# Kernel optimization log

Measured on AMD Instinct MI355X. Metric: run time of the kernel, lower is better.

## Reference

```python
import jax, jax.numpy as jnp
import numpy as np

N_NODES = 100000
N_EDGES = 1600000
IN_DIM = 128
HID = 128
N_CLS = 10
N_GRAPHS = 128


def setup_inputs() -> dict:
    key = jax.random.key(0)
    ks = jax.random.split(key, 8)
    x = jax.random.normal(ks[0], (N_NODES, IN_DIM), dtype=jnp.float32)
    edge_index = jax.random.randint(ks[1], (2, N_EDGES), 0, N_NODES, dtype=jnp.int64)
    batch = jnp.sort(jax.random.randint(ks[2], (N_NODES,), 0, N_GRAPHS, dtype=jnp.int64))
    # GCNConv weights (PyG uses glorot; scale approximated) and biases
    W1 = jax.random.normal(ks[3], (IN_DIM, HID), dtype=jnp.float32) * (1.0 / np.sqrt(IN_DIM))
    b1 = jnp.zeros((HID,), dtype=jnp.float32)
    W2 = jax.random.normal(ks[4], (HID, HID), dtype=jnp.float32) * (1.0 / np.sqrt(HID))
    b2 = jnp.zeros((HID,), dtype=jnp.float32)
    Wlin = jax.random.normal(ks[5], (HID, N_CLS), dtype=jnp.float32) * (1.0 / np.sqrt(HID))
    blin = jnp.zeros((N_CLS,), dtype=jnp.float32)
    return {"x": x, "edge_index": edge_index, "batch": batch,
            "W1": W1, "b1": b1, "W2": W2, "b2": b2, "Wlin": Wlin, "blin": blin}


def _gcn_norm(edge_index, n_nodes):
    # PyG GCNConv default: add self-loops, symmetric D^-1/2 A D^-1/2 normalization
    loop = jnp.arange(n_nodes, dtype=edge_index.dtype)
    row = jnp.concatenate([edge_index[0], loop])  # source nodes
    col = jnp.concatenate([edge_index[1], loop])  # destination nodes
    ones = jnp.ones(col.shape[0], dtype=jnp.float32)
    deg = jax.ops.segment_sum(ones, col, num_segments=n_nodes)
    dinv = jnp.where(deg > 0, jax.lax.rsqrt(deg), 0.0)
    norm = dinv[row] * dinv[col]  # per-edge normalization coefficient
    return row, col, norm


def _gcn_conv(x, W, b, row, col, norm, n_nodes):
    h = x @ W                                   # [N, hid] dense transform first (small hid)
    msg = h[row] * norm[:, None]                # gather + scale over edges
    out = jax.ops.segment_sum(msg, col, num_segments=n_nodes)  # scatter-add aggregation
    return out + b


def reference(x, edge_index, batch, W1, b1, W2, b2, Wlin, blin):
    n = x.shape[0]
    row, col, norm = _gcn_norm(edge_index, n)
    h = jax.nn.relu(_gcn_conv(x, W1, b1, row, col, norm, n))
    h = jax.nn.relu(_gcn_conv(h, W2, b2, row, col, norm, n))
    # global_mean_pool over batch ids
    sums = jax.ops.segment_sum(h, batch, num_segments=N_GRAPHS)
    cnts = jax.ops.segment_sum(jnp.ones((n,), dtype=h.dtype), batch, num_segments=N_GRAPHS)
    pooled = sums / jnp.maximum(cnts, 1.0)[:, None]
    return pooled @ Wlin + blin  # [N_GRAPHS, n_cls]
```

## Files before the change

kernel.cpp:

```cpp
#include <hip/hip_runtime.h>

#define NN 100000
#define NE 1600000
#define DD 128
#define NG 128
#define NC 10
#define AGG_WAVES 8192

#define B1SH 8
#define NB1 ((NN + 255) / 256)
#define EPB 8192
#define NWG1 ((NE + EPB - 1) / EPB)
#define GEMM_BLOCKS ((NN + 63) / 64)

typedef __attribute__((ext_vector_type(8))) short short8v;
typedef __attribute__((ext_vector_type(4))) float f32x4;

__device__ __forceinline__ unsigned short f2bf(float f) {
    unsigned int u = __float_as_uint(f);
    u = (u + 0x7fffu + ((u >> 16) & 1u)) >> 16;
    return (unsigned short)u;
}
__device__ __forceinline__ float bflo(unsigned int p) { return __uint_as_float(p << 16); }
__device__ __forceinline__ float bfhi(unsigned int p) { return __uint_as_float(p & 0xffff0000u); }

template <int IN_BF16>
__device__ __forceinline__ void gemm_body(const void* __restrict__ Xv,
                                          const unsigned short* __restrict__ Wpk,
                                          const float* __restrict__ dinv,
                                          unsigned short* __restrict__ outb, int blk,
                                          unsigned short* wlds) {
    int tid = threadIdx.x;
    const uint4* wg = (const uint4*)Wpk;
    uint4* wl = (uint4*)wlds;
#pragma unroll
    for (int i = 0; i < 8; ++i) wl[tid + i * 256] = wg[tid + i * 256];
    __syncthreads();

    int w = tid >> 6, lane = tid & 63;
    int kg = lane >> 4;
    int rowbase = blk * 64 + w * 16;
    int rl = min(rowbase + (lane & 15), NN - 1);

    short8v a[4];
    if (IN_BF16) {
        const unsigned short* xb = (const unsigned short*)Xv;
#pragma unroll
        for (int kk = 0; kk < 4; ++kk)
            a[kk] = *(const short8v*)(xb + (long)rl * DD + kk * 32 + kg * 8);
    } else {
        const float* xf = (const float*)Xv;
#pragma unroll
        for (int kk = 0; kk < 4; ++kk) {
            float4 f0 = *(const float4*)(xf + (long)rl * DD + kk * 32 + kg * 8);
            float4 f1 = *(const float4*)(xf + (long)rl * DD + kk * 32 + kg * 8 + 4);
            short8v t;
            t[0] = (short)f2bf(f0.x); t[1] = (short)f2bf(f0.y);
            t[2] = (short)f2bf(f0.z); t[3] = (short)f2bf(f0.w);
            t[4] = (short)f2bf(f1.x); t[5] = (short)f2bf(f1.y);
            t[6] = (short)f2bf(f1.z); t[7] = (short)f2bf(f1.w);
            a[kk] = t;
        }
    }

    f32x4 acc[8];
#pragma unroll
    for (int n = 0; n < 8; ++n) acc[n] = (f32x4){0.f, 0.f, 0.f, 0.f};
#pragma unroll
    for (int n = 0; n < 8; ++n) {
#pragma unroll
        for (int kk = 0; kk < 4; ++kk) {
            short8v b = *(const short8v*)(wlds + ((n * 4 + kk) * 64 + lane) * 8);
            acc[n] = __builtin_amdgcn_mfma_f32_16x16x32_bf16(a[kk], b, acc[n], 0, 0, 0);
        }
    }

    int c0 = lane & 15;
#pragma unroll
    for (int reg = 0; reg < 4; ++reg) {
        int row = rowbase + kg * 4 + reg;
        if (row < NN) {
            float dv = dinv[row];
            unsigned short* op = outb + (long)row * DD + c0;
#pragma unroll
            for (int n = 0; n < 8; ++n) op[n * 16] = f2bf(dv * acc[n][reg]);
        }
    }
}

__global__ __launch_bounds__(256) void k1_fused(const int* __restrict__ col, int* __restrict__ hist,
                                                const float* __restrict__ x,
                                                const unsigned short* __restrict__ Wpk1,
                                                unsigned short* __restrict__ hbuf) {
    __shared__ unsigned short wlds[16384];
    int bid = blockIdx.x, t = threadIdx.x;
    if (bid < NWG1) {
        int* lh = (int*)wlds;
        for (int i = t; i < NB1; i += 256) lh[i] = 0;
        __syncthreads();
        int base = bid * EPB;
        int lim = min(base + EPB, NE);
#pragma unroll 4
        for (int e = base + t; e < lim; e += 256) atomicAdd(&lh[col[e] >> B1SH], 1);
        __syncthreads();
        for (int i = t; i < NB1; i += 256) hist[i * NWG1 + bid] = lh[i];
    } else {
        int tid = threadIdx.x;
        const uint4* wg = (const uint4*)Wpk1;
        uint4* wl = (uint4*)wlds;
#pragma unroll
        for (int i = 0; i < 8; ++i) wl[tid + i * 256] = wg[tid + i * 256];
        __syncthreads();
        int w = tid >> 6, lane = tid & 63;
        int kg = lane >> 4;
        int blk = bid - NWG1;
        int rowbase = blk * 64 + w * 16;
        int rl = min(rowbase + (lane & 15), NN - 1);
        short8v a[4];
        const float* xf = x;
#pragma unroll
        for (int kk = 0; kk < 4; ++kk) {
            float4 f0 = *(const float4*)(xf + (long)rl * DD + kk * 32 + kg * 8);
            float4 f1 = *(const float4*)(xf + (long)rl * DD + kk * 32 + kg * 8 + 4);
            short8v tv;
            tv[0] = (short)f2bf(f0.x); tv[1] = (short)f2bf(f0.y);
            tv[2] = (short)f2bf(f0.z); tv[3] = (short)f2bf(f0.w);
            tv[4] = (short)f2bf(f1.x); tv[5] = (short)f2bf(f1.y);
            tv[6] = (short)f2bf(f1.z); tv[7] = (short)f2bf(f1.w);
            a[kk] = tv;
        }
        f32x4 acc[8];
#pragma unroll
        for (int n = 0; n < 8; ++n) acc[n] = (f32x4){0.f, 0.f, 0.f, 0.f};
#pragma unroll
        for (int n = 0; n < 8; ++n) {
#pragma unroll
            for (int kk = 0; kk < 4; ++kk) {
                short8v b = *(const short8v*)(wlds + ((n * 4 + kk) * 64 + lane) * 8);
                acc[n] = __builtin_amdgcn_mfma_f32_16x16x32_bf16(a[kk], b, acc[n], 0, 0, 0);
            }
        }
        int c0 = lane & 15;
#pragma unroll
        for (int reg = 0; reg < 4; ++reg) {
            int row = rowbase + kg * 4 + reg;
            if (row < NN) {
                unsigned short* op = hbuf + (long)row * DD + c0;
#pragma unroll
                for (int n = 0; n < 8; ++n) op[n * 16] = f2bf(acc[n][reg]);
            }
        }
    }
}

__global__ __launch_bounds__(512) void btot_k(const int* __restrict__ hist, int* __restrict__ bbase) {
    __shared__ int tmp[512];
    int t = threadIdx.x;
    int s = 0;
    if (t < NB1) {
        const int* hp = hist + t * NWG1;
        for (int w = 0; w < NWG1; ++w) s += hp[w];
    }
    tmp[t] = s;
    __syncthreads();
    for (int o = 1; o < 512; o <<= 1) {
        int v = (t >= o) ? tmp[t - o] : 0;
        __syncthreads();
        tmp[t] += v;
        __syncthreads();
    }
    if (t < NB1) bbase[t] = tmp[t] - s;
    if (t == 511) bbase[NB1] = tmp[511];
}

__global__ __launch_bounds__(256) void histscan_k(const int* __restrict__ bbase, int* __restrict__ hist) {
    __shared__ int tmp[256];
    int b = blockIdx.x, t = threadIdx.x;
    int v = (t < NWG1) ? hist[b * NWG1 + t] : 0;
    tmp[t] = v;
    __syncthreads();
    for (int o = 1; o < 256; o <<= 1) {
        int u = (t >= o) ? tmp[t - o] : 0;
        __syncthreads();
        tmp[t] += u;
        __syncthreads();
    }
    int excl = tmp[t] - v;
    if (t < NWG1) hist[b * NWG1 + t] = bbase[b] + excl;
}

__global__ __launch_bounds__(256) void part1_k(const int* __restrict__ row, const int* __restrict__ col,
                                               const int* __restrict__ hist, int* __restrict__ tmpe) {
    __shared__ int lcur[NB1];
    int t = threadIdx.x, w = blockIdx.x;
    for (int i = t; i < NB1; i += 256) lcur[i] = hist[i * NWG1 + w];
    __syncthreads();
    int base = w * EPB;
    int lim = min(base + EPB, NE);
#pragma unroll 4
    for (int e = base + t; e < lim; e += 256) {
        int c = col[e];
        int pos = atomicAdd(&lcur[c >> B1SH], 1);
        tmpe[pos] = (row[e] << B1SH) | (c & 255);
    }
}

__global__ __launch_bounds__(512) void part2b_k(const int* __restrict__ bbase, const int* __restrict__ tmpe,
                                                unsigned int* __restrict__ csr_src, int* __restrict__ offs,
                                                float* __restrict__ dinv, unsigned int* __restrict__ hpb) {
    __shared__ int lcnt[256];
    __shared__ int lsc[256];
    int b = blockIdx.x, t = threadIdx.x;
    if (t < 256) lcnt[t] = 0;
    __syncthreads();
    int ebeg = bbase[b], eend = bbase[b + 1];
    for (int e = ebeg + t; e < eend; e += 512) atomicAdd(&lcnt[tmpe[e] & 255], 1);
    __syncthreads();
    if (t < 256) lsc[t] = lcnt[t];
    __syncthreads();
    for (int o = 1; o < 256; o <<= 1) {
        int v = (t < 256 && t >= o) ? lsc[t - o] : 0;
        __syncthreads();
        if (t < 256) lsc[t] += v;
        __syncthreads();
    }
    int n0 = b << B1SH;
    if (t < 256) {
        int c = lcnt[t];
        int excl = lsc[t] - c;
        int node = n0 + t;
        float dvf = rsqrtf((float)c + 1.0f);
        if (node < NN) {
            offs[node] = ebeg + excl;
            dinv[node] = dvf;
        }
        lsc[t] = ebeg + excl;
        ((float*)lcnt)[t] = dvf;
    }
    if (b == NB1 - 1 && t == 0) offs[NN] = NE;
    __syncthreads();
    for (int e = ebeg + t; e < eend; e += 512) {
        int p = tmpe[e];
        int pos = atomicAdd(&lsc[p & 255], 1);
        csr_src[pos] = (unsigned int)(p >> B1SH) << 6;
    }
    int nend = min(n0 + 256, NN);
    unsigned int lane = t & 63;
    for (int r = n0 + (t >> 6); r < nend; r += 8) {
        float dv = ((const float*)lcnt)[r - n0];
        unsigned int p = hpb[(unsigned int)r * 64u + lane];
        hpb[(unsigned int)r * 64u + lane] =
            ((unsigned int)f2bf(dv * bflo(p))) | ((unsigned int)f2bf(dv * bfhi(p)) << 16);
    }
}

__global__ __launch_bounds__(256) void pack_w2_k(const float* __restrict__ W1, const float* __restrict__ W2,
                                                 unsigned short* __restrict__ Wpk1,
                                                 unsigned short* __restrict__ Wpk2,
                                                 float* __restrict__ gsum) {
    int t = threadIdx.x;
    if (blockIdx.x == 2) {
        float4* g4 = (float4*)gsum;
        for (int i = t; i < NG * DD / 4; i += 256) g4[i] = make_float4(0, 0, 0, 0);
        return;
    }
    const float* W = blockIdx.x ? W2 : W1;
    unsigned short* Wpk = blockIdx.x ? Wpk2 : Wpk1;
    for (int f = t * 64; f < t * 64 + 64; ++f) {
        int j = f & 7, lane = (f >> 3) & 63, kk = (f >> 9) & 3, n = f >> 11;
        int k = kk * 32 + ((lane >> 4) << 3) + j;
        int c = n * 16 + (lane & 15);
        Wpk[f] = f2bf(W[k * DD + c]);
    }
}

__global__ __launch_bounds__(256) void gemm2_k(const unsigned short* __restrict__ xb,
                                               const unsigned short* __restrict__ Wpk,
                                               const float* __restrict__ dinv,
                                               unsigned short* __restrict__ outb) {
    __shared__ unsigned short wlds[16384];
    gemm_body<1>(xb, Wpk, dinv, outb, blockIdx.x, wlds);
}

__device__ __forceinline__ void agg_node(const unsigned int* __restrict__ hpb,
                                         const unsigned int* __restrict__ csr,
                                         int s, int e_end, unsigned int lane,
                                         float& accx, float& accy) {
    int e = s;
    for (; e + 16 <= e_end; e += 16) {
        unsigned int p0 = hpb[csr[e] + lane];
        unsigned int p1 = hpb[csr[e + 1] + lane];
        unsigned int p2 = hpb[csr[e + 2] + lane];
        unsigned int p3 = hpb[csr[e + 3] + lane];
        unsigned int p4 = hpb[csr[e + 4] + lane];
        unsigned int p5 = hpb[csr[e + 5] + lane];
        unsigned int p6 = hpb[csr[e + 6] + lane];
        unsigned int p7 = hpb[csr[e + 7] + lane];
        unsigned int q0 = hpb[csr[e + 8] + lane];
        unsigned int q1 = hpb[csr[e + 9] + lane];
        unsigned int q2 = hpb[csr[e + 10] + lane];
        unsigned int q3 = hpb[csr[e + 11] + lane];
        unsigned int q4 = hpb[csr[e + 12] + lane];
        unsigned int q5 = hpb[csr[e + 13] + lane];
        unsigned int q6 = hpb[csr[e + 14] + lane];
        unsigned int q7 = hpb[csr[e + 15] + lane];
        accx += ((bflo(p0) + bflo(p1)) + (bflo(p2) + bflo(p3))) +
                ((bflo(p4) + bflo(p5)) + (bflo(p6) + bflo(p7))) +
                ((bflo(q0) + bflo(q1)) + (bflo(q2) + bflo(q3))) +
                ((bflo(q4) + bflo(q5)) + (bflo(q6) + bflo(q7)));
        accy += ((bfhi(p0) + bfhi(p1)) + (bfhi(p2) + bfhi(p3))) +
                ((bfhi(p4) + bfhi(p5)) + (bfhi(p6) + bfhi(p7))) +
                ((bfhi(q0) + bfhi(q1)) + (bfhi(q2) + bfhi(q3))) +
                ((bfhi(q4) + bfhi(q5)) + (bfhi(q6) + bfhi(q7)));
    }
    if (e + 8 <= e_end) {
        unsigned int p0 = hpb[csr[e] + lane];
        unsigned int p1 = hpb[csr[e + 1] + lane];
        unsigned int p2 = hpb[csr[e + 2] + lane];
        unsigned int p3 = hpb[csr[e + 3] + lane];
        unsigned int p4 = hpb[csr[e + 4] + lane];
        unsigned int p5 = hpb[csr[e + 5] + lane];
        unsigned int p6 = hpb[csr[e + 6] + lane];
        unsigned int p7 = hpb[csr[e + 7] + lane];
        accx += (bflo(p0) + bflo(p1)) + (bflo(p2) + bflo(p3)) +
                (bflo(p4) + bflo(p5)) + (bflo(p6) + bflo(p7));
        accy += (bfhi(p0) + bfhi(p1)) + (bfhi(p2) + bfhi(p3)) +
                (bfhi(p4) + bfhi(p5)) + (bfhi(p6) + bfhi(p7));
        e += 8;
    }
    if (e + 4 <= e_end) {
        unsigned int p0 = hpb[csr[e] + lane];
        unsigned int p1 = hpb[csr[e + 1] + lane];
        unsigned int p2 = hpb[csr[e + 2] + lane];
        unsigned int p3 = hpb[csr[e + 3] + lane];
        accx += (bflo(p0) + bflo(p1)) + (bflo(p2) + bflo(p3));
        accy += (bfhi(p0) + bfhi(p1)) + (bfhi(p2) + bfhi(p3));
        e += 4;
    }
    for (; e < e_end; ++e) {
        unsigned int p0 = hpb[csr[e] + lane];
        accx += bflo(p0);
        accy += bfhi(p0);
    }
}

__global__ __launch_bounds__(256) void agg_k(const unsigned int* __restrict__ hpb,
                                             const float* __restrict__ dinv,
                                             const int* __restrict__ offs,
                                             const unsigned int* __restrict__ csr,
                                             const float* __restrict__ bias,
                                             unsigned short* __restrict__ outb) {
    int wv = (blockIdx.x << 2) + (threadIdx.x >> 6);
    unsigned int lane = threadIdx.x & 63;
    float2 bb = ((const float2*)bias)[lane];
    for (int node = wv; node < NN; node += AGG_WAVES) {
        unsigned int ps = hpb[(unsigned int)node * 64u + lane];
        float accx = bflo(ps), accy = bfhi(ps);
        agg_node(hpb, csr, offs[node], offs[node + 1], lane, accx, accy);
        float dv = dinv[node];
        float ox = fmaxf(fmaf(dv, accx, bb.x), 0.0f);
        float oy = fmaxf(fmaf(dv, accy, bb.y), 0.0f);
        ((ushort2*)outb)[(unsigned int)node * 64u + lane] = make_ushort2(f2bf(ox), f2bf(oy));
    }
}

__global__ __launch_bounds__(256) void agg2pool_k(const unsigned int* __restrict__ hpb,
                                                  const float* __restrict__ dinv,
                                                  const int* __restrict__ offs,
                                                  const unsigned int* __restrict__ csr,
                                                  const float* __restrict__ bias,
                                                  const int* __restrict__ batch,
                                                  float* __restrict__ gsum) {
    int wave = (blockIdx.x << 2) + (threadIdx.x >> 6);
    unsigned int lane = threadIdx.x & 63;
    const int per = (NN + AGG_WAVES - 1) / AGG_WAVES;
    int s = wave * per;
    int e = min(s + per, NN);
    if (s >= e) return;
    float2 bb = ((const float2*)bias)[lane];
    float2 acc = {0.0f, 0.0f};
    int cur = batch[s];
    for (int node = s; node < e; ++node) {
        int bg = batch[node];
        if (bg != cur) {
            atomicAdd(&gsum[cur * DD + 2 * lane], acc.x);
            atomicAdd(&gsum[cur * DD + 2 * lane + 1], acc.y);
            acc.x = 0.0f; acc.y = 0.0f;
            cur = bg;
        }
        unsigned int ps = hpb[(unsigned int)node * 64u + lane];
        float accx = bflo(ps), accy = bfhi(ps);
        agg_node(hpb, csr, offs[node], offs[node + 1], lane, accx, accy);
        float dv = dinv[node];
        acc.x += fmaxf(fmaf(dv, accx, bb.x), 0.0f);
        acc.y += fmaxf(fmaf(dv, accy, bb.y), 0.0f);
    }
    atomicAdd(&gsum[cur * DD + 2 * lane], acc.x);
    atomicAdd(&gsum[cur * DD + 2 * lane + 1], acc.y);
}

__global__ __launch_bounds__(256) void final_k(const float* __restrict__ gsum, const int* __restrict__ batch,
                                               const float* __restrict__ Wlin, const float* __restrict__ blin,
                                               float* __restrict__ out) {
    int idx = blockIdx.x * 256 + threadIdx.x;
    if (idx >= NG * NC) return;
    int g = idx / NC, c = idx % NC;
    int s0, s1;
    {
        int lo = 0, hi = NN;
        while (lo < hi) { int m = (lo + hi) >> 1; if (batch[m] < g) lo = m + 1; else hi = m; }
        s0 = lo;
        lo = s0; hi = NN;
        while (lo < hi) { int m = (lo + hi) >> 1; if (batch[m] < g + 1) lo = m + 1; else hi = m; }
        s1 = lo;
    }
    int cnt = s1 - s0;
    float inv = 1.0f / fmaxf((float)cnt, 1.0f);
    float acc = blin[c];
    for (int k = 0; k < DD; ++k) acc = fmaf(gsum[g * DD + k] * inv, Wlin[k * NC + c], acc);
    out[idx] = acc;
}

extern "C" void kernel_launch(void* const* d_in, const int* in_sizes, int n_in,
                              void* d_out, int out_size, void* d_ws, size_t ws_size,
                              hipStream_t stream) {
    const float* x     = (const float*)d_in[0];
    const int*   ei    = (const int*)d_in[1];
    const int*   batch = (const int*)d_in[2];
    const float* W1    = (const float*)d_in[3];
    const float* b1    = (const float*)d_in[4];
    const float* W2    = (const float*)d_in[5];
    const float* b2    = (const float*)d_in[6];
    const float* Wlin  = (const float*)d_in[7];
    const float* blin  = (const float*)d_in[8];
    float* out = (float*)d_out;

    const int* erow = ei;
    const int* ecol = ei + NE;

    char* ws = (char*)d_ws;
    size_t off = 0;
    auto alloc = [&](size_t bytes) {
        void* p = ws + off;
        off = (off + bytes + 255) & ~(size_t)255;
        return p;
    };
    unsigned short* hbuf  = (unsigned short*)alloc((size_t)NN * DD * 2);
    unsigned short* habuf = (unsigned short*)alloc((size_t)NN * DD * 2);
    unsigned short* Wpk1  = (unsigned short*)alloc(16384 * 2);
    unsigned short* Wpk2  = (unsigned short*)alloc(16384 * 2);
    float* dinv     = (float*)alloc(NN * 4);
    int*   offs     = (int*)alloc((NN + 1) * 4);
    int*   bbase    = (int*)alloc((NB1 + 1) * 4);
    int*   hist     = (int*)alloc((size_t)NB1 * NWG1 * 4);
    int*   tmpe     = (int*)alloc((size_t)NE * 4);
    unsigned int* csrsrc = (unsigned int*)alloc((size_t)NE * 4);
    float* gsum     = (float*)alloc(NG * DD * 4);
    (void)ws_size; (void)in_sizes; (void)n_in; (void)out_size;

    pack_w2_k<<<3, 256, 0, stream>>>(W1, W2, Wpk1, Wpk2, gsum);
    k1_fused<<<NWG1 + GEMM_BLOCKS, 256, 0, stream>>>(ecol, hist, x, Wpk1, hbuf);
    btot_k<<<1, 512, 0, stream>>>(hist, bbase);
    histscan_k<<<NB1, 256, 0, stream>>>(bbase, hist);
    part1_k<<<NWG1, 256, 0, stream>>>(erow, ecol, hist, tmpe);
    part2b_k<<<NB1, 512, 0, stream>>>(bbase, tmpe, csrsrc, offs, dinv, (unsigned int*)hbuf);

    agg_k<<<AGG_WAVES / 4, 256, 0, stream>>>((const unsigned int*)hbuf, dinv, offs, csrsrc, b1, habuf);
    gemm2_k<<<GEMM_BLOCKS, 256, 0, stream>>>(habuf, Wpk2, dinv, hbuf);
    agg2pool_k<<<AGG_WAVES / 4, 256, 0, stream>>>((const unsigned int*)hbuf, dinv, offs, csrsrc, b2,
                                                  batch, gsum);
    final_k<<<(NG * NC + 255) / 256, 256, 0, stream>>>(gsum, batch, Wlin, blin, out);
}
```

Before: 240.8 us.

## Merge weight packing into histogram kernel and move GEMM1 into partition kernel

Weight packing and gsum zeroing now run as extra blocks of the histogram kernel, which drops one launch. The first-layer GEMM moves out of the histogram kernel and runs alongside the edge partition pass. Both passes are memory-bound, so this rebalances work across launches so each overlaps better. The partition kernel now carries 32KB of LDS for every block, which may reduce occupancy for its scatter blocks.

```diff
diff --git a/kernel.cpp b/kernel.cpp
--- a/kernel.cpp
+++ b/kernel.cpp
@@ -24,45 +24,32 @@
 __device__ __forceinline__ float bflo(unsigned int p) { return __uint_as_float(p << 16); }
 __device__ __forceinline__ float bfhi(unsigned int p) { return __uint_as_float(p & 0xffff0000u); }
 
-template <int IN_BF16>
-__device__ __forceinline__ void gemm_body(const void* __restrict__ Xv,
-                                          const unsigned short* __restrict__ Wpk,
-                                          const float* __restrict__ dinv,
-                                          unsigned short* __restrict__ outb, int blk,
-                                          unsigned short* wlds) {
+__device__ __forceinline__ void gemm1_body(const float* __restrict__ x,
+                                           const unsigned short* __restrict__ Wpk1,
+                                           unsigned short* __restrict__ hbuf, int blk,
+                                           unsigned short* wlds) {
     int tid = threadIdx.x;
-    const uint4* wg = (const uint4*)Wpk;
+    const uint4* wg = (const uint4*)Wpk1;
     uint4* wl = (uint4*)wlds;
 #pragma unroll
     for (int i = 0; i < 8; ++i) wl[tid + i * 256] = wg[tid + i * 256];
     __syncthreads();
-
     int w = tid >> 6, lane = tid & 63;
     int kg = lane >> 4;
     int rowbase = blk * 64 + w * 16;
     int rl = min(rowbase + (lane & 15), NN - 1);
-
     short8v a[4];
-    if (IN_BF16) {
-        const unsigned short* xb = (const unsigned short*)Xv;
-#pragma unroll
-        for (int kk = 0; kk < 4; ++kk)
-            a[kk] = *(const short8v*)(xb + (long)rl * DD + kk * 32 + kg * 8);
-    } else {
-        const float* xf = (const float*)Xv;
-#pragma unroll
-        for (int kk = 0; kk < 4; ++kk) {
-            float4 f0 = *(const float4*)(xf + (long)rl * DD + kk * 32 + kg * 8);
-            float4 f1 = *(const float4*)(xf + (long)rl * DD + kk * 32 + kg * 8 + 4);
-            short8v t;
-            t[0] = (short)f2bf(f0.x); t[1] = (short)f2bf(f0.y);
-            t[2] = (short)f2bf(f0.z); t[3] = (short)f2bf(f0.w);
-            t[4] = (short)f2bf(f1.x); t[5] = (short)f2bf(f1.y);
-            t[6] = (short)f2bf(f1.z); t[7] = (short)f2bf(f1.w);
-            a[kk] = t;
-        }
-    }
-
+#pragma unroll
+    for (int kk = 0; kk < 4; ++kk) {
+        float4 f0 = *(const float4*)(x + (long)rl * DD + kk * 32 + kg * 8);
+        float4 f1 = *(const float4*)(x + (long)rl * DD + kk * 32 + kg * 8 + 4);
+        short8v tv;
+        tv[0] = (short)f2bf(f0.x); tv[1] = (short)f2bf(f0.y);
+        tv[2] = (short)f2bf(f0.z); tv[3] = (short)f2bf(f0.w);
+        tv[4] = (short)f2bf(f1.x); tv[5] = (short)f2bf(f1.y);
+        tv[6] = (short)f2bf(f1.z); tv[7] = (short)f2bf(f1.w);
+        a[kk] = tv;
+    }
     f32x4 acc[8];
 #pragma unroll
     for (int n = 0; n < 8; ++n) acc[n] = (f32x4){0.f, 0.f, 0.f, 0.f};
@@ -74,28 +61,26 @@
             acc[n] = __builtin_amdgcn_mfma_f32_16x16x32_bf16(a[kk], b, acc[n], 0, 0, 0);
         }
     }
-
     int c0 = lane & 15;
 #pragma unroll
     for (int reg = 0; reg < 4; ++reg) {
         int row = rowbase + kg * 4 + reg;
         if (row < NN) {
-            float dv = dinv[row];
-            unsigned short* op = outb + (long)row * DD + c0;
-#pragma unroll
-            for (int n = 0; n < 8; ++n) op[n * 16] = f2bf(dv * acc[n][reg]);
-        }
-    }
-}
-
-__global__ __launch_bounds__(256) void k1_fused(const int* __restrict__ col, int* __restrict__ hist,
-                                                const float* __restrict__ x,
-                                                const unsigned short* __restrict__ Wpk1,
-                                                unsigned short* __restrict__ hbuf) {
-    __shared__ unsigned short wlds[16384];
+            unsigned short* op = hbuf + (long)row * DD + c0;
+#pragma unroll
+            for (int n = 0; n < 8; ++n) op[n * 16] = f2bf(acc[n][reg]);
+        }
+    }
+}
+
+__global__ __launch_bounds__(256) void k0_fused(const int* __restrict__ col, int* __restrict__ hist,
+                                                const float* __restrict__ W1, const float* __restrict__ W2,
+                                                unsigned short* __restrict__ Wpk1,
+                                                unsigned short* __restrict__ Wpk2,
+                                                float* __restrict__ gsum) {
+    __shared__ int lh[NB1];
     int bid = blockIdx.x, t = threadIdx.x;
     if (bid < NWG1) {
-        int* lh = (int*)wlds;
         for (int i = t; i < NB1; i += 256) lh[i] = 0;
         __syncthreads();
         int base = bid * EPB;
@@ -104,51 +89,17 @@
         for (int e = base + t; e < lim; e += 256) atomicAdd(&lh[col[e] >> B1SH], 1);
         __syncthreads();
         for (int i = t; i < NB1; i += 256) hist[i * NWG1 + bid] = lh[i];
+    } else if (bid == NWG1 + 2) {
+        float4* g4 = (float4*)gsum;
+        for (int i = t; i < NG * DD / 4; i += 256) g4[i] = make_float4(0, 0, 0, 0);
     } else {
-        int tid = threadIdx.x;
-        const uint4* wg = (const uint4*)Wpk1;
-        uint4* wl = (uint4*)wlds;
-#pragma unroll
-        for (int i = 0; i < 8; ++i) wl[tid + i * 256] = wg[tid + i * 256];
-        __syncthreads();
-        int w = tid >> 6, lane = tid & 63;
-        int kg = lane >> 4;
-        int blk = bid - NWG1;
-        int rowbase = blk * 64 + w * 16;
-        int rl = min(rowbase + (lane & 15), NN - 1);
-        short8v a[4];
-        const float* xf = x;
-#pragma unroll
-        for (int kk = 0; kk < 4; ++kk) {
-            float4 f0 = *(const float4*)(xf + (long)rl * DD + kk * 32 + kg * 8);
-            float4 f1 = *(const float4*)(xf + (long)rl * DD + kk * 32 + kg * 8 + 4);
-            short8v tv;
-            tv[0] = (short)f2bf(f0.x); tv[1] = (short)f2bf(f0.y);
-            tv[2] = (short)f2bf(f0.z); tv[3] = (short)f2bf(f0.w);
-            tv[4] = (short)f2bf(f1.x); tv[5] = (short)f2bf(f1.y);
-            tv[6] = (short)f2bf(f1.z); tv[7] = (short)f2bf(f1.w);
-            a[kk] = tv;
-        }
-        f32x4 acc[8];
-#pragma unroll
-        for (int n = 0; n < 8; ++n) acc[n] = (f32x4){0.f, 0.f, 0.f, 0.f};
-#pragma unroll
-        for (int n = 0; n < 8; ++n) {
-#pragma unroll
-            for (int kk = 0; kk < 4; ++kk) {
-                short8v b = *(const short8v*)(wlds + ((n * 4 + kk) * 64 + lane) * 8);
-                acc[n] = __builtin_amdgcn_mfma_f32_16x16x32_bf16(a[kk], b, acc[n], 0, 0, 0);
-            }
-        }
-        int c0 = lane & 15;
-#pragma unroll
-        for (int reg = 0; reg < 4; ++reg) {
-            int row = rowbase + kg * 4 + reg;
-            if (row < NN) {
-                unsigned short* op = hbuf + (long)row * DD + c0;
-#pragma unroll
-                for (int n = 0; n < 8; ++n) op[n * 16] = f2bf(acc[n][reg]);
-            }
+        const float* W = (bid == NWG1) ? W1 : W2;
+        unsigned short* Wpk = (bid == NWG1) ? Wpk1 : Wpk2;
+        for (int f = t * 64; f < t * 64 + 64; ++f) {
+            int j = f & 7, lane = (f >> 3) & 63, kk = (f >> 9) & 3, n = f >> 11;
+            int k = kk * 32 + ((lane >> 4) << 3) + j;
+            int c = n * 16 + (lane & 15);
+            Wpk[f] = f2bf(W[k * DD + c]);
         }
     }
 }
@@ -189,19 +140,27 @@
     if (t < NWG1) hist[b * NWG1 + t] = bbase[b] + excl;
 }
 
-__global__ __launch_bounds__(256) void part1_k(const int* __restrict__ row, const int* __restrict__ col,
-                                               const int* __restrict__ hist, int* __restrict__ tmpe) {
-    __shared__ int lcur[NB1];
-    int t = threadIdx.x, w = blockIdx.x;
-    for (int i = t; i < NB1; i += 256) lcur[i] = hist[i * NWG1 + w];
-    __syncthreads();
-    int base = w * EPB;
-    int lim = min(base + EPB, NE);
+__global__ __launch_bounds__(256) void k3_fused(const int* __restrict__ row, const int* __restrict__ col,
+                                                const int* __restrict__ hist, int* __restrict__ tmpe,
+                                                const float* __restrict__ x,
+                                                const unsigned short* __restrict__ Wpk1,
+                                                unsigned short* __restrict__ hbuf) {
+    __shared__ unsigned short wlds[16384];
+    int bid = blockIdx.x, t = threadIdx.x;
+    if (bid < NWG1) {
+        int* lcur = (int*)wlds;
+        for (int i = t; i < NB1; i += 256) lcur[i] = hist[i * NWG1 + bid];
+        __syncthreads();
+        int base = bid * EPB;
+        int lim = min(base + EPB, NE);
 #pragma unroll 4
-    for (int e = base + t; e < lim; e += 256) {
-        int c = col[e];
-        int pos = atomicAdd(&lcur[c >> B1SH], 1);
-        tmpe[pos] = (row[e] << B1SH) | (c & 255);
+        for (int e = base + t; e < lim; e += 256) {
+            int c = col[e];
+            int pos = atomicAdd(&lcur[c >> B1SH], 1);
+            tmpe[pos] = (row[e] << B1SH) | (c & 255);
+        }
+    } else {
+        gemm1_body(x, Wpk1, hbuf, bid - NWG1, wlds);
     }
 }
 
@@ -254,32 +213,47 @@
     }
 }
 
-__global__ __launch_bounds__(256) void pack_w2_k(const float* __restrict__ W1, const float* __restrict__ W2,
-                                                 unsigned short* __restrict__ Wpk1,
-                                                 unsigned short* __restrict__ Wpk2,
-                                                 float* __restrict__ gsum) {
-    int t = threadIdx.x;
-    if (blockIdx.x == 2) {
-        float4* g4 = (float4*)gsum;
-        for (int i = t; i < NG * DD / 4; i += 256) g4[i] = make_float4(0, 0, 0, 0);
-        return;
-    }
-    const float* W = blockIdx.x ? W2 : W1;
-    unsigned short* Wpk = blockIdx.x ? Wpk2 : Wpk1;
-    for (int f = t * 64; f < t * 64 + 64; ++f) {
-        int j = f & 7, lane = (f >> 3) & 63, kk = (f >> 9) & 3, n = f >> 11;
-        int k = kk * 32 + ((lane >> 4) << 3) + j;
-        int c = n * 16 + (lane & 15);
-        Wpk[f] = f2bf(W[k * DD + c]);
-    }
-}
-
 __global__ __launch_bounds__(256) void gemm2_k(const unsigned short* __restrict__ xb,
                                                const unsigned short* __restrict__ Wpk,
                                                const float* __restrict__ dinv,
                                                unsigned short* __restrict__ outb) {
     __shared__ unsigned short wlds[16384];
-    gemm_body<1>(xb, Wpk, dinv, outb, blockIdx.x, wlds);
+    int tid = threadIdx.x;
+    const uint4* wg = (const uint4*)Wpk;
+    uint4* wl = (uint4*)wlds;
+#pragma unroll
+    for (int i = 0; i < 8; ++i) wl[tid + i * 256] = wg[tid + i * 256];
+    __syncthreads();
+    int w = tid >> 6, lane = tid & 63;
+    int kg = lane >> 4;
+    int rowbase = blockIdx.x * 64 + w * 16;
+    int rl = min(rowbase + (lane & 15), NN - 1);
+    short8v a[4];
+#pragma unroll
+    for (int kk = 0; kk < 4; ++kk)
+        a[kk] = *(const short8v*)(xb + (long)rl * DD + kk * 32 + kg * 8);
+    f32x4 acc[8];
+#pragma unroll
+    for (int n = 0; n < 8; ++n) acc[n] = (f32x4){0.f, 0.f, 0.f, 0.f};
+#pragma unroll
+    for (int n = 0; n < 8; ++n) {
+#pragma unroll
+        for (int kk = 0; kk < 4; ++kk) {
+            short8v b = *(const short8v*)(wlds + ((n * 4 + kk) * 64 + lane) * 8);
+            acc[n] = __builtin_amdgcn_mfma_f32_16x16x32_bf16(a[kk], b, acc[n], 0, 0, 0);
+        }
+    }
+    int c0 = lane & 15;
+#pragma unroll
+    for (int reg = 0; reg < 4; ++reg) {
+        int row = rowbase + kg * 4 + reg;
+        if (row < NN) {
+            float dv = dinv[row];
+            unsigned short* op = outb + (long)row * DD + c0;
+#pragma unroll
+            for (int n = 0; n < 8; ++n) op[n * 16] = f2bf(dv * acc[n][reg]);
+        }
+    }
 }
 
 __device__ __forceinline__ void agg_node(const unsigned int* __restrict__ hpb,
@@ -458,11 +432,10 @@
     float* gsum     = (float*)alloc(NG * DD * 4);
     (void)ws_size; (void)in_sizes; (void)n_in; (void)out_size;
 
-    pack_w2_k<<<3, 256, 0, stream>>>(W1, W2, Wpk1, Wpk2, gsum);
-    k1_fused<<<NWG1 + GEMM_BLOCKS, 256, 0, stream>>>(ecol, hist, x, Wpk1, hbuf);
+    k0_fused<<<NWG1 + 3, 256, 0, stream>>>(ecol, hist, W1, W2, Wpk1, Wpk2, gsum);
     btot_k<<<1, 512, 0, stream>>>(hist, bbase);
     histscan_k<<<NB1, 256, 0, stream>>>(bbase, hist);
-    part1_k<<<NWG1, 256, 0, stream>>>(erow, ecol, hist, tmpe);
+    k3_fused<<<NWG1 + GEMM_BLOCKS, 256, 0, stream>>>(erow, ecol, hist, tmpe, x, Wpk1, hbuf);
     part2b_k<<<NB1, 512, 0, stream>>>(bbase, tmpe, csrsrc, offs, dinv, (unsigned int*)hbuf);
 
     agg_k<<<AGG_WAVES / 4, 256, 0, stream>>>((const unsigned int*)hbuf, dinv, offs, csrsrc, b1, habuf);
```

Result: faster. 231.7 us (-3.8%).
